# Kernel tuning notes

Hardware: AMD Instinct MI355X
Metric: run time of the kernel (lower is better)

The kernel has to match this reference:

```python
import jax, jax.numpy as jnp
import numpy as np

B, E, LC, LE, D = 32, 8, 256, 512, 256   # batch, evi_num, claim_len, evidence_len, emb_dim
OUT, H = 128, 1                          # attention hidden dim, head_num
NEG = -1e18


def setup_inputs() -> dict:
    key = jax.random.key(0)
    ks = jax.random.split(key, 8)
    claim = jax.random.normal(ks[0], (B, E, LC, D), jnp.float32)
    evidence = jax.random.normal(ks[1], (B, E, LE, D), jnp.float32)
    claim_len_mask = jax.random.randint(ks[2], (B, E, 1, LC), 0, 2).astype(jnp.int32)
    evidence_len_mask = jax.random.randint(ks[3], (B, E, 1, LE), 0, 2).astype(jnp.int32)
    s2d = 1.0 / np.sqrt(2 * D)
    so = 1.0 / np.sqrt(OUT)
    W1 = jax.random.normal(ks[4], (2 * D, OUT), jnp.float32) * s2d  # torch W1.weight.T
    w2 = jax.random.normal(ks[5], (OUT, H), jnp.float32) * so
    W2 = jax.random.normal(ks[6], (2 * D, OUT), jnp.float32) * s2d
    w1 = jax.random.normal(ks[7], (OUT, H), jnp.float32) * so
    return {"claim": claim, "claim_len_mask": claim_len_mask,
            "evidence": evidence, "evidence_len_mask": evidence_len_mask,
            "W1": W1, "w2": w2, "W2": W2, "w1": w1}


def _pooled_attend(seq, seq_mask, pooled, W, w):
    # seq: (B,E,L,D), pooled: (B,E,1,D), W: (2D,OUT), w: (OUT,H)
    # cat([seq, pooled_expanded]) @ W  ==  seq @ W[:D] + pooled @ W[D:]  (broadcast)
    h = jnp.tanh(seq @ W[:D] + pooled @ W[D:])          # (B,E,L,OUT)
    att = h @ w                                          # (B,E,L,H)
    mask = jnp.swapaxes(seq_mask, -1, -2).astype(bool)   # (B,E,L,1), broadcast over H
    att = jnp.where(mask, att, NEG)
    scores = jax.nn.softmax(att, axis=-2)                # softmax over L
    out = jnp.einsum('belh,beld->behd', scores, seq)     # (B,E,H,D)
    return out.reshape(out.shape[0], out.shape[1], 1, -1)  # (B,E,1,H*D)


def reference(claim, claim_len_mask, evidence, evidence_len_mask, W1, w2, W2, w1):
    c_mean = jnp.mean(claim, axis=-2, keepdims=True)     # (B,E,1,D)
    e_hat = _pooled_attend(evidence, evidence_len_mask, c_mean, W1, w2)
    e_mean = jnp.mean(evidence, axis=-2, keepdims=True)  # (B,E,1,D)
    c_hat = _pooled_attend(claim, claim_len_mask, e_mean, W2, w1)
    return c_hat, e_hat
```

## Files before the change

### kernel.cpp

```cpp
#include <hip/hip_runtime.h>
#include <hip/hip_bf16.h>
#include <math.h>

#define BE   256
#define DIM  256
#define OUTD 128
#define LCL  256
#define LEV  512
#define NEGV -1e18f

typedef short  bf16x8  __attribute__((ext_vector_type(8)));
typedef float  floatx4 __attribute__((ext_vector_type(4)));

union BF1 { __hip_bfloat16 h; unsigned short u; };
union BF2 { __hip_bfloat162 h; unsigned int u; };

__device__ __forceinline__ float fast_tanh(float x) {
    float xc = fminf(fmaxf(x, -15.f), 15.f);
    float e = __expf(2.f * xc);
    return (e - 1.f) * __builtin_amdgcn_rcpf(e + 1.f);
}

__global__ __launch_bounds__(256) void k_meanprep(
    const float* __restrict__ claim, const float* __restrict__ evidence,
    const float* __restrict__ W1, const float* __restrict__ W2,
    float* __restrict__ partial,
    unsigned short* __restrict__ WT1, unsigned short* __restrict__ WT2)
{
    const int b = blockIdx.x;
    const int t = threadIdx.x;
    if (b >= 3072) {
        const int idx = b - 3072;
        const int side = idx >> 7;
        const int n = idx & 127;
        const float* W = side ? W2 : W1;
        unsigned short* WT = side ? WT2 : WT1;
        BF1 c; c.h = __float2bfloat16(W[(size_t)t * OUTD + n]);
        WT[n * DIM + t] = c.u;
        return;
    }
    const int pair = b / 12;
    const int chunk = b % 12;
    const float* src = (chunk < 4)
        ? claim + ((size_t)pair * LCL + chunk * 64) * DIM
        : evidence + ((size_t)pair * LEV + (chunk - 4) * 64) * DIM;
    float s = 0.f;
#pragma unroll
    for (int r = 0; r < 64; ++r) s += src[r * DIM + t];
    partial[(size_t)b * DIM + t] = s;
}

__global__ __launch_bounds__(512) void k_redbias(
    const float* __restrict__ partial,
    const float* __restrict__ W1, const float* __restrict__ W2,
    float* __restrict__ bias_e, float* __restrict__ bias_c)
{
    const int pair = blockIdx.x;
    const int t = threadIdx.x;
    __shared__ float sm[2][DIM];
    __shared__ float sb[2][2][OUTD];
    if (t < 256) {
        float s = 0.f;
#pragma unroll
        for (int j = 0; j < 4; ++j) s += partial[((size_t)pair * 12 + j) * DIM + t];
        sm[0][t] = s * (1.f / LCL);
    } else {
        const int t2 = t - 256;
        float s = 0.f;
#pragma unroll
        for (int j = 4; j < 12; ++j) s += partial[((size_t)pair * 12 + j) * DIM + t2];
        sm[1][t2] = s * (1.f / LEV);
    }
    __syncthreads();
    const int side = t >> 8, o = t & 127, dh = (t >> 7) & 1;
    const float* W = side ? W2 : W1;
    const float* m = sm[side];
    float s = 0.f;
#pragma unroll 8
    for (int i = 0; i < 128; ++i) {
        const int d = dh * 128 + i;
        s += m[d] * W[(size_t)(DIM + d) * OUTD + o];
    }
    sb[side][dh][o] = s;
    __syncthreads();
    if (t < 256) {
        const int sd = t >> 7, oo = t & 127;
        const float bv = sb[sd][0][oo] + sb[sd][1][oo];
        (sd ? bias_c : bias_e)[pair * OUTD + oo] = bv;
    }
}

template <int L>
__global__ __launch_bounds__(256) void k_att(
    const float* __restrict__ seq, const unsigned short* __restrict__ WT,
    const float* __restrict__ wvec, const float* __restrict__ bias,
    float* __restrict__ att)
{
    constexpr int SAPC = 136;
    __shared__ unsigned short sA[128 * SAPC];
    __shared__ float sred[128][2];

    const int pair = blockIdx.x;
    const int rowbase = blockIdx.y * 128;
    const int t = threadIdx.x;
    const int lane = t & 63;
    const int wv = t >> 6;
    const int wrow = wv >> 1, wcolg = wv & 1;
    const int q = lane >> 4, c16 = lane & 15;

    const float4* sp4 = (const float4*)(seq + ((size_t)pair * L + rowbase) * DIM);

    floatx4 acc[4][4];
#pragma unroll
    for (int ra = 0; ra < 4; ++ra)
#pragma unroll
        for (int ct = 0; ct < 4; ++ct) acc[ra][ct] = (floatx4){0.f, 0.f, 0.f, 0.f};

    const unsigned short* wbase = WT + (size_t)(wcolg * 64 + c16) * DIM + q * 8;
    bf16x8 bcur[4], bnxt[4];
#pragma unroll
    for (int ct = 0; ct < 4; ++ct)
        bcur[ct] = *(const bf16x8*)(wbase + ct * 16 * DIM);

    for (int kc = 0; kc < 2; ++kc) {
        __syncthreads();
#pragma unroll
        for (int i = 0; i < 16; ++i) {
            const int idx = t + i * 256;
            const int row = idx >> 5;
            const int f4 = idx & 31;
            const float4 v = sp4[row * 64 + kc * 32 + f4];
            BF2 lo, hi;
            lo.h = __float22bfloat162_rn(make_float2(v.x, v.y));
            hi.h = __float22bfloat162_rn(make_float2(v.z, v.w));
            *(uint2*)&sA[row * SAPC + f4 * 4] = make_uint2(lo.u, hi.u);
        }
        __syncthreads();
#pragma unroll
        for (int ks4 = 0; ks4 < 4; ++ks4) {
            const int ks = kc * 4 + ks4;
            if (ks < 7) {
#pragma unroll
                for (int ct = 0; ct < 4; ++ct)
                    bnxt[ct] = *(const bf16x8*)(wbase + ct * 16 * DIM + (ks + 1) * 32);
            }
            bf16x8 af[4];
#pragma unroll
            for (int ra = 0; ra < 4; ++ra)
                af[ra] = *(const bf16x8*)&sA[(wrow * 64 + ra * 16 + c16) * SAPC + ks4 * 32 + q * 8];
#pragma unroll
            for (int ra = 0; ra < 4; ++ra)
#pragma unroll
                for (int ct = 0; ct < 4; ++ct)
                    acc[ra][ct] = __builtin_amdgcn_mfma_f32_16x16x32_bf16(af[ra], bcur[ct], acc[ra][ct], 0, 0, 0);
#pragma unroll
            for (int ct = 0; ct < 4; ++ct) bcur[ct] = bnxt[ct];
        }
    }

    float bc[4], wc[4];
#pragma unroll
    for (int ct = 0; ct < 4; ++ct) {
        const int col = wcolg * 64 + ct * 16 + c16;
        bc[ct] = bias[pair * OUTD + col];
        wc[ct] = wvec[col];
    }
#pragma unroll
    for (int ra = 0; ra < 4; ++ra) {
#pragma unroll
        for (int reg = 0; reg < 4; ++reg) {
            float s = 0.f;
#pragma unroll
            for (int ct = 0; ct < 4; ++ct)
                s += fast_tanh(acc[ra][ct][reg] + bc[ct]) * wc[ct];
#pragma unroll
            for (int off = 1; off < 16; off <<= 1) s += __shfl_xor(s, off, 64);
            if (c16 == 0)
                sred[wrow * 64 + ra * 16 + q * 4 + reg][wcolg] = s;
        }
    }
    __syncthreads();
    if (t < 128)
        att[(size_t)pair * L + rowbase + t] = sred[t][0] + sred[t][1];
}

template <int L>
__global__ __launch_bounds__(1024) void k_soft(
    const float* __restrict__ seq, const int* __restrict__ mask,
    const float* __restrict__ att, float* __restrict__ outp)
{
    const int pair = blockIdx.x;
    const int t = threadIdx.x;
    __shared__ float p[L];
    __shared__ float red[8];
    __shared__ float4 red2[16][64];

    float lmax = -INFINITY;
    if (t < 256) {
#pragma unroll
        for (int k = 0; k < L / 256; ++k) {
            const int i = t + k * 256;
            float a = att[(size_t)pair * L + i];
            a = mask[pair * L + i] ? a : NEGV;
            p[i] = a;
            lmax = fmaxf(lmax, a);
        }
#pragma unroll
        for (int off = 32; off > 0; off >>= 1) lmax = fmaxf(lmax, __shfl_xor(lmax, off, 64));
        if ((t & 63) == 0) red[t >> 6] = lmax;
    }
    __syncthreads();
    if (t < 256) {
        const float gmax = fmaxf(fmaxf(red[0], red[1]), fmaxf(red[2], red[3]));
        float lsum = 0.f;
#pragma unroll
        for (int k = 0; k < L / 256; ++k) {
            const int i = t + k * 256;
            const float e = expf(p[i] - gmax);
            p[i] = e;
            lsum += e;
        }
#pragma unroll
        for (int off = 32; off > 0; off >>= 1) lsum += __shfl_xor(lsum, off, 64);
        if ((t & 63) == 0) red[4 + (t >> 6)] = lsum;
    }
    __syncthreads();

    const int d4 = t & 63, lg = t >> 6;
    constexpr int LC = L / 16;
    const float4* sp4 = (const float4*)(seq + (size_t)pair * L * DIM);
    float4 o = make_float4(0.f, 0.f, 0.f, 0.f);
    for (int l = lg * LC; l < (lg + 1) * LC; ++l) {
        const float pl = p[l];
        const float4 v = sp4[l * 64 + d4];
        o.x += pl * v.x; o.y += pl * v.y; o.z += pl * v.z; o.w += pl * v.w;
    }
    red2[lg][d4] = o;
    __syncthreads();
    if (t < 64) {
        float4 s = make_float4(0.f, 0.f, 0.f, 0.f);
#pragma unroll
        for (int j = 0; j < 16; ++j) {
            const float4 v = red2[j][t];
            s.x += v.x; s.y += v.y; s.z += v.z; s.w += v.w;
        }
        const float inv = 1.f / (red[4] + red[5] + red[6] + red[7]);
        ((float4*)(outp + (size_t)pair * DIM))[t] =
            make_float4(s.x * inv, s.y * inv, s.z * inv, s.w * inv);
    }
}

extern "C" void kernel_launch(void* const* d_in, const int* in_sizes, int n_in,
                              void* d_out, int out_size, void* d_ws, size_t ws_size,
                              hipStream_t stream) {
    const float* claim    = (const float*)d_in[0];
    const int*   cmask    = (const int*)  d_in[1];
    const float* evidence = (const float*)d_in[2];
    const int*   emask    = (const int*)  d_in[3];
    const float* W1       = (const float*)d_in[4];
    const float* w2       = (const float*)d_in[5];
    const float* W2       = (const float*)d_in[6];
    const float* w1       = (const float*)d_in[7];
    float* out = (float*)d_out;

    float* ws = (float*)d_ws;
    float* partial = ws;
    float* bias_e  = partial + 3072 * DIM;
    float* bias_c  = bias_e + BE * OUTD;
    float* att_e   = bias_c + BE * OUTD;
    float* att_c   = att_e + BE * LEV;
    unsigned short* WT1 = (unsigned short*)(att_c + BE * LCL);
    unsigned short* WT2 = WT1 + OUTD * DIM;

    k_meanprep<<<3328, 256, 0, stream>>>(claim, evidence, W1, W2, partial, WT1, WT2);
    k_redbias<<<BE, 512, 0, stream>>>(partial, W1, W2, bias_e, bias_c);
    k_att<LEV><<<dim3(BE, 4), 256, 0, stream>>>(evidence, WT1, w2, bias_e, att_e);
    k_att<LCL><<<dim3(BE, 2), 256, 0, stream>>>(claim, WT2, w1, bias_c, att_c);
    k_soft<LEV><<<BE, 1024, 0, stream>>>(evidence, emask, att_e, out + BE * DIM);
    k_soft<LCL><<<BE, 1024, 0, stream>>>(claim, cmask, att_c, out);
}
```

Baseline: 345.9 us.

## Fuse attention scoring and softmax-pooling into one online-softmax kernel per pair

```diff
diff --git a/kernel.cpp b/kernel.cpp
--- a/kernel.cpp
+++ b/kernel.cpp
@@ -41,13 +41,28 @@
     }
     const int pair = b / 12;
     const int chunk = b % 12;
-    const float* src = (chunk < 4)
+    const float4* src4 = (const float4*)((chunk < 4)
         ? claim + ((size_t)pair * LCL + chunk * 64) * DIM
-        : evidence + ((size_t)pair * LEV + (chunk - 4) * 64) * DIM;
-    float s = 0.f;
-#pragma unroll
-    for (int r = 0; r < 64; ++r) s += src[r * DIM + t];
-    partial[(size_t)b * DIM + t] = s;
+        : evidence + ((size_t)pair * LEV + (chunk - 4) * 64) * DIM);
+    const int col4 = t & 63;
+    const int rgrp = t >> 6;
+    float4 a = make_float4(0.f, 0.f, 0.f, 0.f);
+#pragma unroll
+    for (int r = 0; r < 16; ++r) {
+        const float4 v = src4[(rgrp * 16 + r) * 64 + col4];
+        a.x += v.x; a.y += v.y; a.z += v.z; a.w += v.w;
+    }
+    __shared__ float4 sm4[4][64];
+    sm4[rgrp][col4] = a;
+    __syncthreads();
+    if (t < 64) {
+        const float4 s0 = sm4[0][t], s1 = sm4[1][t], s2 = sm4[2][t], s3 = sm4[3][t];
+        ((float4*)(partial + (size_t)b * DIM))[t] =
+            make_float4(s0.x + s1.x + s2.x + s3.x,
+                        s0.y + s1.y + s2.y + s3.y,
+                        s0.z + s1.z + s2.z + s3.z,
+                        s0.w + s1.w + s2.w + s3.w);
+    }
 }
 
 __global__ __launch_bounds__(512) void k_redbias(
@@ -90,164 +105,149 @@
     }
 }
 
-template <int L>
-__global__ __launch_bounds__(256) void k_att(
-    const float* __restrict__ seq, const unsigned short* __restrict__ WT,
-    const float* __restrict__ wvec, const float* __restrict__ bias,
-    float* __restrict__ att)
+__global__ __launch_bounds__(512, 4) void k_fused(
+    const float* __restrict__ claim, const float* __restrict__ evidence,
+    const unsigned short* __restrict__ WT1, const unsigned short* __restrict__ WT2,
+    const float* __restrict__ w2v, const float* __restrict__ w1v,
+    const float* __restrict__ bias_e, const float* __restrict__ bias_c,
+    const int* __restrict__ emask, const int* __restrict__ cmask,
+    float* __restrict__ out)
 {
-    constexpr int SAPC = 136;
+    constexpr int SAPC = 264;
     __shared__ unsigned short sA[128 * SAPC];
     __shared__ float sred[128][2];
-
-    const int pair = blockIdx.x;
-    const int rowbase = blockIdx.y * 128;
+    __shared__ float patt[128];
+    __shared__ float rmax[2], rsum[2];
+    __shared__ float ofin[256];
+
+    const int bid = blockIdx.x;
+    const bool is_ev = bid < BE;
+    const int pair = bid & (BE - 1);
+    const float* __restrict__ seq  = is_ev ? evidence : claim;
+    const unsigned short* __restrict__ WT = is_ev ? WT1 : WT2;
+    const float* __restrict__ wvec = is_ev ? w2v : w1v;
+    const float* __restrict__ bias = is_ev ? bias_e : bias_c;
+    const int*   __restrict__ mask = is_ev ? emask : cmask;
+    float* __restrict__ outp       = is_ev ? out + (size_t)BE * DIM : out;
+    const int L  = is_ev ? LEV : LCL;
+    const int NT = L >> 7;
+
     const int t = threadIdx.x;
     const int lane = t & 63;
     const int wv = t >> 6;
-    const int wrow = wv >> 1, wcolg = wv & 1;
+    const int wrow = wv >> 1;
+    const int wcolg = wv & 1;
     const int q = lane >> 4, c16 = lane & 15;
-
-    const float4* sp4 = (const float4*)(seq + ((size_t)pair * L + rowbase) * DIM);
-
-    floatx4 acc[4][4];
-#pragma unroll
-    for (int ra = 0; ra < 4; ++ra)
-#pragma unroll
-        for (int ct = 0; ct < 4; ++ct) acc[ra][ct] = (floatx4){0.f, 0.f, 0.f, 0.f};
-
+    const int d = t & 255, rg = t >> 8;
+
+    float bc[4], wc[4];
+#pragma unroll
+    for (int ct = 0; ct < 4; ++ct) {
+        const int col = wcolg * 64 + ct * 16 + c16;
+        bc[ct] = bias[pair * OUTD + col];
+        wc[ct] = wvec[col];
+    }
     const unsigned short* wbase = WT + (size_t)(wcolg * 64 + c16) * DIM + q * 8;
-    bf16x8 bcur[4], bnxt[4];
-#pragma unroll
-    for (int ct = 0; ct < 4; ++ct)
-        bcur[ct] = *(const bf16x8*)(wbase + ct * 16 * DIM);
-
-    for (int kc = 0; kc < 2; ++kc) {
-        __syncthreads();
-#pragma unroll
+
+    float Oacc = 0.f;
+    float m_run = -INFINITY, l_run = 0.f;
+
+    for (int tile = 0; tile < NT; ++tile) {
+        const float4* sp4 = (const float4*)(seq + ((size_t)pair * L + tile * 128) * DIM);
+#pragma unroll 8
         for (int i = 0; i < 16; ++i) {
-            const int idx = t + i * 256;
-            const int row = idx >> 5;
-            const int f4 = idx & 31;
-            const float4 v = sp4[row * 64 + kc * 32 + f4];
+            const int idx = t + i * 512;
+            const float4 v = sp4[idx];
+            const int row = idx >> 6, f4 = idx & 63;
             BF2 lo, hi;
             lo.h = __float22bfloat162_rn(make_float2(v.x, v.y));
             hi.h = __float22bfloat162_rn(make_float2(v.z, v.w));
             *(uint2*)&sA[row * SAPC + f4 * 4] = make_uint2(lo.u, hi.u);
         }
         __syncthreads();
-#pragma unroll
-        for (int ks4 = 0; ks4 < 4; ++ks4) {
-            const int ks = kc * 4 + ks4;
+
+        floatx4 acc[2][4];
+#pragma unroll
+        for (int ra = 0; ra < 2; ++ra)
+#pragma unroll
+            for (int ct = 0; ct < 4; ++ct) acc[ra][ct] = (floatx4){0.f, 0.f, 0.f, 0.f};
+        bf16x8 bcur[4], bnxt[4];
+#pragma unroll
+        for (int ct = 0; ct < 4; ++ct)
+            bcur[ct] = *(const bf16x8*)(wbase + (size_t)ct * 16 * DIM);
+#pragma unroll
+        for (int ks = 0; ks < 8; ++ks) {
             if (ks < 7) {
 #pragma unroll
                 for (int ct = 0; ct < 4; ++ct)
-                    bnxt[ct] = *(const bf16x8*)(wbase + ct * 16 * DIM + (ks + 1) * 32);
+                    bnxt[ct] = *(const bf16x8*)(wbase + (size_t)ct * 16 * DIM + (ks + 1) * 32);
             }
-            bf16x8 af[4];
-#pragma unroll
-            for (int ra = 0; ra < 4; ++ra)
-                af[ra] = *(const bf16x8*)&sA[(wrow * 64 + ra * 16 + c16) * SAPC + ks4 * 32 + q * 8];
-#pragma unroll
-            for (int ra = 0; ra < 4; ++ra)
+            bf16x8 af[2];
+#pragma unroll
+            for (int ra = 0; ra < 2; ++ra)
+                af[ra] = *(const bf16x8*)&sA[(wrow * 32 + ra * 16 + c16) * SAPC + ks * 32 + q * 8];
+#pragma unroll
+            for (int ra = 0; ra < 2; ++ra)
 #pragma unroll
                 for (int ct = 0; ct < 4; ++ct)
                     acc[ra][ct] = __builtin_amdgcn_mfma_f32_16x16x32_bf16(af[ra], bcur[ct], acc[ra][ct], 0, 0, 0);
 #pragma unroll
             for (int ct = 0; ct < 4; ++ct) bcur[ct] = bnxt[ct];
         }
-    }
-
-    float bc[4], wc[4];
-#pragma unroll
-    for (int ct = 0; ct < 4; ++ct) {
-        const int col = wcolg * 64 + ct * 16 + c16;
-        bc[ct] = bias[pair * OUTD + col];
-        wc[ct] = wvec[col];
-    }
-#pragma unroll
-    for (int ra = 0; ra < 4; ++ra) {
-#pragma unroll
-        for (int reg = 0; reg < 4; ++reg) {
-            float s = 0.f;
-#pragma unroll
-            for (int ct = 0; ct < 4; ++ct)
-                s += fast_tanh(acc[ra][ct][reg] + bc[ct]) * wc[ct];
-#pragma unroll
-            for (int off = 1; off < 16; off <<= 1) s += __shfl_xor(s, off, 64);
-            if (c16 == 0)
-                sred[wrow * 64 + ra * 16 + q * 4 + reg][wcolg] = s;
-        }
-    }
-    __syncthreads();
-    if (t < 128)
-        att[(size_t)pair * L + rowbase + t] = sred[t][0] + sred[t][1];
-}
-
-template <int L>
-__global__ __launch_bounds__(1024) void k_soft(
-    const float* __restrict__ seq, const int* __restrict__ mask,
-    const float* __restrict__ att, float* __restrict__ outp)
-{
-    const int pair = blockIdx.x;
-    const int t = threadIdx.x;
-    __shared__ float p[L];
-    __shared__ float red[8];
-    __shared__ float4 red2[16][64];
-
-    float lmax = -INFINITY;
-    if (t < 256) {
-#pragma unroll
-        for (int k = 0; k < L / 256; ++k) {
-            const int i = t + k * 256;
-            float a = att[(size_t)pair * L + i];
-            a = mask[pair * L + i] ? a : NEGV;
-            p[i] = a;
-            lmax = fmaxf(lmax, a);
-        }
-#pragma unroll
-        for (int off = 32; off > 0; off >>= 1) lmax = fmaxf(lmax, __shfl_xor(lmax, off, 64));
-        if ((t & 63) == 0) red[t >> 6] = lmax;
-    }
-    __syncthreads();
-    if (t < 256) {
-        const float gmax = fmaxf(fmaxf(red[0], red[1]), fmaxf(red[2], red[3]));
-        float lsum = 0.f;
-#pragma unroll
-        for (int k = 0; k < L / 256; ++k) {
-            const int i = t + k * 256;
-            const float e = expf(p[i] - gmax);
-            p[i] = e;
-            lsum += e;
-        }
-#pragma unroll
-        for (int off = 32; off > 0; off >>= 1) lsum += __shfl_xor(lsum, off, 64);
-        if ((t & 63) == 0) red[4 + (t >> 6)] = lsum;
-    }
-    __syncthreads();
-
-    const int d4 = t & 63, lg = t >> 6;
-    constexpr int LC = L / 16;
-    const float4* sp4 = (const float4*)(seq + (size_t)pair * L * DIM);
-    float4 o = make_float4(0.f, 0.f, 0.f, 0.f);
-    for (int l = lg * LC; l < (lg + 1) * LC; ++l) {
-        const float pl = p[l];
-        const float4 v = sp4[l * 64 + d4];
-        o.x += pl * v.x; o.y += pl * v.y; o.z += pl * v.z; o.w += pl * v.w;
-    }
-    red2[lg][d4] = o;
-    __syncthreads();
-    if (t < 64) {
-        float4 s = make_float4(0.f, 0.f, 0.f, 0.f);
-#pragma unroll
-        for (int j = 0; j < 16; ++j) {
-            const float4 v = red2[j][t];
-            s.x += v.x; s.y += v.y; s.z += v.z; s.w += v.w;
-        }
-        const float inv = 1.f / (red[4] + red[5] + red[6] + red[7]);
-        ((float4*)(outp + (size_t)pair * DIM))[t] =
-            make_float4(s.x * inv, s.y * inv, s.z * inv, s.w * inv);
-    }
+
+#pragma unroll
+        for (int ra = 0; ra < 2; ++ra) {
+#pragma unroll
+            for (int reg = 0; reg < 4; ++reg) {
+                float s = 0.f;
+#pragma unroll
+                for (int ct = 0; ct < 4; ++ct)
+                    s += fast_tanh(acc[ra][ct][reg] + bc[ct]) * wc[ct];
+#pragma unroll
+                for (int off = 1; off < 16; off <<= 1) s += __shfl_xor(s, off, 64);
+                if (c16 == 0)
+                    sred[wrow * 32 + ra * 16 + q * 4 + reg][wcolg] = s;
+            }
+        }
+        __syncthreads();
+
+        if (t < 128) {
+            float a = sred[t][0] + sred[t][1];
+            a = mask[pair * L + tile * 128 + t] ? a : NEGV;
+            patt[t] = a;
+            float mx = a;
+#pragma unroll
+            for (int off = 1; off < 64; off <<= 1) mx = fmaxf(mx, __shfl_xor(mx, off, 64));
+            if (lane == 0) rmax[wv] = mx;
+        }
+        __syncthreads();
+        const float newm = fmaxf(m_run, fmaxf(rmax[0], rmax[1]));
+        const float scale = expf(m_run - newm);
+        if (t < 128) {
+            const float e = expf(patt[t] - newm);
+            patt[t] = e;
+            float sm = e;
+#pragma unroll
+            for (int off = 1; off < 64; off <<= 1) sm += __shfl_xor(sm, off, 64);
+            if (lane == 0) rsum[wv] = sm;
+        }
+        __syncthreads();
+        l_run = l_run * scale + rsum[0] + rsum[1];
+        m_run = newm;
+        Oacc *= scale;
+
+        const float* sp = seq + ((size_t)pair * L + tile * 128 + rg * 64) * DIM + d;
+#pragma unroll 8
+        for (int r = 0; r < 64; ++r)
+            Oacc += patt[rg * 64 + r] * sp[(size_t)r * DIM];
+    }
+
+    if (rg == 0) ofin[d] = Oacc;
+    __syncthreads();
+    if (rg == 1) ofin[d] += Oacc;
+    __syncthreads();
+    if (t < 256)
+        outp[(size_t)pair * DIM + t] = ofin[t] / l_run;
 }
 
 extern "C" void kernel_launch(void* const* d_in, const int* in_sizes, int n_in,
@@ -267,15 +267,11 @@
     float* partial = ws;
     float* bias_e  = partial + 3072 * DIM;
     float* bias_c  = bias_e + BE * OUTD;
-    float* att_e   = bias_c + BE * OUTD;
-    float* att_c   = att_e + BE * LEV;
-    unsigned short* WT1 = (unsigned short*)(att_c + BE * LCL);
+    unsigned short* WT1 = (unsigned short*)(bias_c + BE * OUTD);
     unsigned short* WT2 = WT1 + OUTD * DIM;
 
     k_meanprep<<<3328, 256, 0, stream>>>(claim, evidence, W1, W2, partial, WT1, WT2);
     k_redbias<<<BE, 512, 0, stream>>>(partial, W1, W2, bias_e, bias_c);
-    k_att<LEV><<<dim3(BE, 4), 256, 0, stream>>>(evidence, WT1, w2, bias_e, att_e);
-    k_att<LCL><<<dim3(BE, 2), 256, 0, stream>>>(claim, WT2, w1, bias_c, att_c);
-    k_soft<LEV><<<BE, 1024, 0, stream>>>(evidence, emask, att_e, out + BE * DIM);
-    k_soft<LCL><<<BE, 1024, 0, stream>>>(claim, cmask, att_c, out);
-}
+    k_fused<<<512, 512, 0, stream>>>(claim, evidence, WT1, WT2, w2, w1,
+                                     bias_e, bias_c, emask, cmask, out);
+}
```

Result: slower. 461.5 us (+33.4%).
